# Kernel tuning notes

Hardware: AMD Instinct MI355X
Metric: run time of the kernel (lower is better)

The kernel has to match this reference:

```python
import jax, jax.numpy as jnp
import numpy as np

N_NODES = 50000
N_EDGES = 800000
IN_C = 128
OUT_C = 128
ALPHA = 0.2  # leaky_relu negative slope (args.egat_alpha)
EDGE_K = 3   # edgefeat width, fixed by W_out in-dim = 3*out_channels


def setup_inputs() -> dict:
    key = jax.random.key(0)
    k = jax.random.split(key, 7)
    h = jax.random.normal(k[0], (N_NODES, IN_C), dtype=jnp.float32)
    edge_index = jax.random.randint(k[1], (2, N_EDGES), 0, N_NODES, dtype=jnp.int64)
    edgefeat = jax.random.uniform(k[2], (N_EDGES, EDGE_K), dtype=jnp.float32)
    # glorot-initialized linear weights (stored as [in, out] for x @ W)
    def glorot(kk, fan_in, fan_out):
        lim = jnp.sqrt(6.0 / (fan_in + fan_out)).astype(jnp.float32)
        return jax.random.uniform(kk, (fan_in, fan_out), jnp.float32, -lim, lim)
    W = glorot(k[3], IN_C, OUT_C)
    a1 = glorot(k[4], OUT_C, 1)
    a2 = glorot(k[5], OUT_C, 1)
    W_out = glorot(k[6], EDGE_K * OUT_C, OUT_C)
    return {"h": h, "edge_index": edge_index, "edgefeat": edgefeat,
            "W": W, "a1": a1, "a2": a2, "W_out": W_out}


def reference(h, edge_index, edgefeat, W, a1, a2, W_out):
    src = edge_index[0]  # j: message source
    dst = edge_index[1]  # i: aggregation target
    n = h.shape[0]

    Wh = h @ W                                   # [N, C]
    s1 = Wh @ a1                                 # [N, 1] alpha_j scores
    s2 = Wh @ a2                                 # [N, 1] alpha_i scores

    # edge_update: leaky_relu(alpha_j + alpha_i) * edge_attr, then edge softmax over dst
    e = s1[src] + s2[dst]                        # [E, 1]
    e = jnp.where(e >= 0, e, ALPHA * e)
    alpha = e * edgefeat                         # [E, 3]
    m = jax.ops.segment_max(alpha, dst, num_segments=n)      # [N, 3]
    m = jnp.where(jnp.isfinite(m), m, 0.0)
    ex = jnp.exp(alpha - m[dst])
    denom = jax.ops.segment_sum(ex, dst, num_segments=n)     # [N, 3]
    att = ex / (denom[dst] + 1e-16)              # [E, 3] (dropout p applied at eval -> identity)

    # message: outer product att[E,3] x x_j[E,C] -> [E, 3C] -> W_out -> [E, C]
    x_j = Wh[src]                                # [E, C]
    msg = (att[:, :, None] * x_j[:, None, :]).reshape(att.shape[0], EDGE_K * Wh.shape[1])
    msg = msg @ W_out                            # [E, C]

    # aggregate: sum at destination nodes
    out = jax.ops.segment_sum(msg, dst, num_segments=n)      # [N, C]
    return out
```

## Files before the change

kernel.cpp:

```cpp
#include <hip/hip_runtime.h>
#include <hip/hip_bf16.h>

#define ALPHA 0.2f
typedef unsigned int uint32;
typedef __attribute__((ext_vector_type(8))) short short8;
typedef __attribute__((ext_vector_type(4))) float f32x4;

static __device__ __forceinline__ unsigned short f2bf(float f) {
    unsigned int u = __float_as_uint(f);
    u += 0x7fffu + ((u >> 16) & 1u);
    return (unsigned short)(u >> 16);
}
static __device__ __forceinline__ uint32 pk2bf(float lo, float hi) {
    return (uint32)f2bf(lo) | ((uint32)f2bf(hi) << 16);
}
static __device__ __forceinline__ float bflo(uint32 u) { return __uint_as_float(u << 16); }
static __device__ __forceinline__ float bfhi(uint32 u) { return __uint_as_float(u & 0xffff0000u); }

__global__ __launch_bounds__(256) void k1_hist_prep(const int* __restrict__ ei,
                                                    int* __restrict__ counts,
                                                    int* __restrict__ eslot, int E,
                                                    const float* __restrict__ W,
                                                    const float* __restrict__ Wout,
                                                    const float* __restrict__ a1,
                                                    const float* __restrict__ a2,
                                                    unsigned short* __restrict__ WT2,
                                                    float* __restrict__ w1f,
                                                    float* __restrict__ w2f, int nbh) {
    __shared__ float Wos[128 * 16];
    const int tid = threadIdx.x;
    if ((int)blockIdx.x < nbh) {
        int e = blockIdx.x * 256 + tid;
        if (e < E) eslot[e] = atomicAdd(&counts[ei[E + e]], 1);
        return;
    }
    int bp = blockIdx.x - nbh;
    if (bp < 24) {
        int s = bp >> 3, nb = bp & 7;
        for (int i = tid; i < 2048; i += 256) {
            int c = i >> 4, q = i & 15;
            Wos[i] = Wout[(size_t)(s * 128 + c) * 128 + nb * 16 + q];
        }
        __syncthreads();
        int j = tid & 127, nh = tid >> 7;
        float acc[8];
#pragma unroll
        for (int p = 0; p < 8; ++p) acc[p] = 0.f;
        for (int c = 0; c < 128; ++c) {
            float w = W[j * 128 + c];
#pragma unroll
            for (int p = 0; p < 8; ++p) acc[p] += w * Wos[c * 16 + nh * 8 + p];
        }
#pragma unroll
        for (int p = 0; p < 8; ++p) {
            int n = nb * 16 + nh * 8 + p;
            WT2[((size_t)s * 128 + n) * 128 + j] = f2bf(acc[p]);
        }
    } else {
        if (tid < 128) {
            float acc1 = 0.f, acc2 = 0.f;
            for (int c = 0; c < 128; ++c) {
                float w = W[tid * 128 + c];
                acc1 += w * a1[c];
                acc2 += w * a2[c];
            }
            w1f[tid] = acc1;
            w2f[tid] = acc2;
        }
    }
}

__global__ __launch_bounds__(256) void k2_mmy_scan(const float* __restrict__ h,
                                                   const unsigned short* __restrict__ WT2,
                                                   const float* __restrict__ w1f,
                                                   const float* __restrict__ w2f,
                                                   unsigned short* __restrict__ Yb,
                                                   float* __restrict__ s1,
                                                   float* __restrict__ s2, int M,
                                                   const int* __restrict__ counts,
                                                   int* __restrict__ rowptr,
                                                   int N, int E, int nbm) {
    __shared__ unsigned short As[64 * 128];
    __shared__ unsigned short Bs[128 * 128];
    __shared__ float ws1[128], ws2[128];
    __shared__ int wsums[4];
    __shared__ int base_s;
    const int tid = threadIdx.x;

    if ((int)blockIdx.x >= nbm) {
        const int bs   = blockIdx.x - nbm;
        const int lane = tid & 63, wv = tid >> 6;
        const int limit = bs * 1024;
        int acc = 0;
        for (int i = tid * 4; i < limit; i += 1024) {
            int4 v = *(const int4*)(counts + i);
            acc += v.x + v.y + v.z + v.w;
        }
#pragma unroll
        for (int off = 32; off > 0; off >>= 1) acc += __shfl_down(acc, off);
        if (lane == 0) wsums[wv] = acc;
        __syncthreads();
        if (tid == 0) base_s = wsums[0] + wsums[1] + wsums[2] + wsums[3];
        __syncthreads();
        int i0 = bs * 1024 + tid * 4;
        int v0 = 0, v1 = 0, v2 = 0, v3 = 0;
        if (i0 + 3 < N) {
            int4 v = *(const int4*)(counts + i0);
            v0 = v.x; v1 = v.y; v2 = v.z; v3 = v.w;
        } else {
            if (i0 + 0 < N) v0 = counts[i0 + 0];
            if (i0 + 1 < N) v1 = counts[i0 + 1];
            if (i0 + 2 < N) v2 = counts[i0 + 2];
            if (i0 + 3 < N) v3 = counts[i0 + 3];
        }
        int tt = v0 + v1 + v2 + v3;
        int incl = tt;
#pragma unroll
        for (int off = 1; off < 64; off <<= 1) {
            int t = __shfl_up(incl, off);
            if (lane >= off) incl += t;
        }
        __syncthreads();
        if (lane == 63) wsums[wv] = incl;
        __syncthreads();
        int woff = 0;
        for (int w2 = 0; w2 < wv; ++w2) woff += wsums[w2];
        int base = base_s + woff + (incl - tt);
        if (i0 + 0 < N) rowptr[i0 + 0] = base;
        if (i0 + 1 < N) rowptr[i0 + 1] = base + v0;
        if (i0 + 2 < N) rowptr[i0 + 2] = base + v0 + v1;
        if (i0 + 3 < N) rowptr[i0 + 3] = base + v0 + v1 + v2;
        if (bs == 0 && tid == 0) rowptr[N] = E;
        return;
    }

    const int lane = tid & 63;
    const int w    = tid >> 6;
    const int row0 = blockIdx.x * 64;

    if (tid < 128) ws1[tid] = w1f[tid];
    else           ws2[tid - 128] = w2f[tid - 128];
    __syncthreads();

    const float4* h4 = (const float4*)h;
    float sp1[4], sp2[4];
#pragma unroll
    for (int m = 0; m < 4; ++m) { sp1[m] = 0.f; sp2[m] = 0.f; }
#pragma unroll
    for (int m = 0; m < 4; ++m) {
        int i = m * 256 + tid;
        int r = i >> 4, g = i & 15;
        int rg = row0 + r;
        float4 va = make_float4(0.f, 0.f, 0.f, 0.f), vb = va;
        if (rg < M) {
            va = h4[(size_t)rg * 32 + g * 2];
            vb = h4[(size_t)rg * 32 + g * 2 + 1];
        }
        float4 wa1 = *(const float4*)(ws1 + g * 8);
        float4 wb1 = *(const float4*)(ws1 + g * 8 + 4);
        float4 wa2 = *(const float4*)(ws2 + g * 8);
        float4 wb2 = *(const float4*)(ws2 + g * 8 + 4);
        sp1[m] += va.x * wa1.x + va.y * wa1.y + va.z * wa1.z + va.w * wa1.w
                + vb.x * wb1.x + vb.y * wb1.y + vb.z * wb1.z + vb.w * wb1.w;
        sp2[m] += va.x * wa2.x + va.y * wa2.y + va.z * wa2.z + va.w * wa2.w
                + vb.x * wb2.x + vb.y * wb2.y + vb.z * wb2.z + vb.w * wb2.w;
        uint4 u;
        u.x = pk2bf(va.x, va.y); u.y = pk2bf(va.z, va.w);
        u.z = pk2bf(vb.x, vb.y); u.w = pk2bf(vb.z, vb.w);
        *(uint4*)(As + r * 128 + ((g ^ (r & 15)) * 8)) = u;
    }
#pragma unroll
    for (int m = 0; m < 4; ++m) {
#pragma unroll
        for (int off = 1; off < 16; off <<= 1) {
            sp1[m] += __shfl_xor(sp1[m], off);
            sp2[m] += __shfl_xor(sp2[m], off);
        }
    }
    if ((tid & 15) == 0) {
#pragma unroll
        for (int m = 0; m < 4; ++m) {
            int rg = row0 + m * 16 + (tid >> 4);
            if (rg < M) { s1[rg] = sp1[m]; s2[rg] = sp2[m]; }
        }
    }

    const int ml   = lane & 15;
    const int quad = lane >> 4;
    for (int ks = 0; ks < 3; ++ks) {
        __syncthreads();
#pragma unroll
        for (int m = 0; m < 8; ++m) {
            int i = m * 256 + tid;
            int n = i >> 4, g = i & 15;
            uint4 v = *(const uint4*)(WT2 + (size_t)ks * 16384 + n * 128 + g * 8);
            *(uint4*)(Bs + n * 128 + ((g ^ (n & 15)) * 8)) = v;
        }
        __syncthreads();

        f32x4 acc[8];
#pragma unroll
        for (int nt = 0; nt < 8; ++nt) acc[nt] = (f32x4){0.f, 0.f, 0.f, 0.f};
#pragma unroll
        for (int kc = 0; kc < 4; ++kc) {
            int gl = ((kc * 4 + quad) ^ ml) * 8;
            short8 af = *(const short8*)(As + (w * 16 + ml) * 128 + gl);
#pragma unroll
            for (int nt = 0; nt < 8; ++nt) {
                short8 bf = *(const short8*)(Bs + (nt * 16 + ml) * 128 + gl);
                acc[nt] = __builtin_amdgcn_mfma_f32_16x16x32_bf16(af, bf, acc[nt], 0, 0, 0);
            }
        }
        int rbase = row0 + w * 16 + quad * 4;
#pragma unroll
        for (int r = 0; r < 4; ++r) {
            int rg = rbase + r;
            if (rg >= M) continue;
            unsigned short* yrow = Yb + (size_t)rg * 384 + ks * 128 + ml;
#pragma unroll
            for (int nt = 0; nt < 8; ++nt)
                yrow[nt * 16] = f2bf(acc[nt][r]);
        }
    }
}

__global__ __launch_bounds__(256) void scatter_kernel(const int* __restrict__ ei,
                                                      const float* __restrict__ ef,
                                                      const float* __restrict__ s1,
                                                      const float* __restrict__ s2,
                                                      const int* __restrict__ rowptr,
                                                      const int* __restrict__ eslot,
                                                      float4* __restrict__ rec, int E) {
    int e = blockIdx.x * blockDim.x + threadIdx.x;
    if (e >= E) return;
    int src = ei[e];
    int dst = ei[E + e];
    float s = s1[src] + s2[dst];
    s = (s >= 0.f) ? s : ALPHA * s;
    float ex0 = __expf(s * ef[e * 3 + 0]);
    float ex1 = __expf(s * ef[e * 3 + 1]);
    float ex2 = __expf(s * ef[e * 3 + 2]);
    int pos = rowptr[dst] + eslot[e];
    rec[pos] = make_float4(ex0, ex1, ex2, __int_as_float(src));
}

__global__ __launch_bounds__(256) void agg_kernel(const float4* __restrict__ rec,
                                                  const int* __restrict__ rowptr,
                                                  const uint32* __restrict__ Yu,
                                                  float* __restrict__ out, int N) {
    int node = (blockIdx.x * blockDim.x + threadIdx.x) >> 6;
    int lane = threadIdx.x & 63;
    if (node >= N) return;
    int beg = rowptr[node], end = rowptr[node + 1];

    float d0 = 0.f, d1 = 0.f, d2 = 0.f;
    for (int jb = beg + lane; jb < end; jb += 64) {
        float4 r = rec[jb];
        d0 += r.x; d1 += r.y; d2 += r.z;
    }
#pragma unroll
    for (int off = 32; off > 0; off >>= 1) {
        d0 += __shfl_xor(d0, off);
        d1 += __shfl_xor(d1, off);
        d2 += __shfl_xor(d2, off);
    }
    float inv0 = 1.f / (d0 + 1e-16f);
    float inv1 = 1.f / (d1 + 1e-16f);
    float inv2 = 1.f / (d2 + 1e-16f);

    float a0 = 0.f, a1 = 0.f;
    int j = beg;
    for (; j + 3 < end; j += 4) {
        float4 r0 = rec[j], r1 = rec[j + 1], r2 = rec[j + 2], r3 = rec[j + 3];
        const uint32* p0 = Yu + (size_t)__float_as_int(r0.w) * 192;
        const uint32* p1 = Yu + (size_t)__float_as_int(r1.w) * 192;
        const uint32* p2 = Yu + (size_t)__float_as_int(r2.w) * 192;
        const uint32* p3 = Yu + (size_t)__float_as_int(r3.w) * 192;
        uint32 u00 = p0[lane], u01 = p0[64 + lane], u02 = p0[128 + lane];
        uint32 u10 = p1[lane], u11 = p1[64 + lane], u12 = p1[128 + lane];
        uint32 u20 = p2[lane], u21 = p2[64 + lane], u22 = p2[128 + lane];
        uint32 u30 = p3[lane], u31 = p3[64 + lane], u32 = p3[128 + lane];
        float w00 = r0.x * inv0, w01 = r0.y * inv1, w02 = r0.z * inv2;
        float w10 = r1.x * inv0, w11 = r1.y * inv1, w12 = r1.z * inv2;
        float w20 = r2.x * inv0, w21 = r2.y * inv1, w22 = r2.z * inv2;
        float w30 = r3.x * inv0, w31 = r3.y * inv1, w32 = r3.z * inv2;
        a0 += w00 * bflo(u00) + w01 * bflo(u01) + w02 * bflo(u02);
        a1 += w00 * bfhi(u00) + w01 * bfhi(u01) + w02 * bfhi(u02);
        a0 += w10 * bflo(u10) + w11 * bflo(u11) + w12 * bflo(u12);
        a1 += w10 * bfhi(u10) + w11 * bfhi(u11) + w12 * bfhi(u12);
        a0 += w20 * bflo(u20) + w21 * bflo(u21) + w22 * bflo(u22);
        a1 += w20 * bfhi(u20) + w21 * bfhi(u21) + w22 * bfhi(u22);
        a0 += w30 * bflo(u30) + w31 * bflo(u31) + w32 * bflo(u32);
        a1 += w30 * bfhi(u30) + w31 * bfhi(u31) + w32 * bfhi(u32);
    }
    for (; j < end; ++j) {
        float4 r0 = rec[j];
        const uint32* p0 = Yu + (size_t)__float_as_int(r0.w) * 192;
        uint32 u00 = p0[lane], u01 = p0[64 + lane], u02 = p0[128 + lane];
        float w00 = r0.x * inv0, w01 = r0.y * inv1, w02 = r0.z * inv2;
        a0 += w00 * bflo(u00) + w01 * bflo(u01) + w02 * bflo(u02);
        a1 += w00 * bfhi(u00) + w01 * bfhi(u01) + w02 * bfhi(u02);
    }
    ((float2*)(out + (size_t)node * 128))[lane] = make_float2(a0, a1);
}

extern "C" void kernel_launch(void* const* d_in, const int* in_sizes, int n_in,
                              void* d_out, int out_size, void* d_ws, size_t ws_size,
                              hipStream_t stream) {
    const float* h    = (const float*)d_in[0];
    const int*   ei   = (const int*)d_in[1];
    const float* ef   = (const float*)d_in[2];
    const float* W    = (const float*)d_in[3];
    const float* a1   = (const float*)d_in[4];
    const float* a2   = (const float*)d_in[5];
    const float* Wout = (const float*)d_in[6];
    float*       out  = (float*)d_out;

    const int N = in_sizes[0] / 128;
    const int E = in_sizes[2] / 3;
    const int nchunk = (N + 1023) / 1024;
    const int nbh    = (E + 255) / 256;
    const int nbm    = (N + 63) / 64;

    float4* rec = (float4*)d_ws;
    unsigned short* Yb  = (unsigned short*)(rec + E);
    unsigned short* WT2 = Yb + (size_t)N * 384;
    float* w1f  = (float*)(WT2 + 3 * 128 * 128);
    float* w2f  = w1f + 128;
    float* s1   = w2f + 128;
    float* s2   = s1 + N;
    int* counts = (int*)(s2 + N);
    int* rowptr = counts + N;
    int* eslot  = rowptr + N + 1;

    (void)hipMemsetAsync(counts, 0, (size_t)N * sizeof(int), stream);

    k1_hist_prep<<<nbh + 25, 256, 0, stream>>>(ei, counts, eslot, E,
                                               W, Wout, a1, a2, WT2, w1f, w2f, nbh);
    k2_mmy_scan<<<nbm + nchunk, 256, 0, stream>>>(h, WT2, w1f, w2f, Yb, s1, s2, N,
                                                  counts, rowptr, N, E, nbm);
    scatter_kernel<<<(E + 255) / 256, 256, 0, stream>>>(ei, ef, s1, s2, rowptr, eslot, rec, E);
    agg_kernel<<<(N * 64 + 255) / 256, 256, 0, stream>>>(rec, rowptr, (const uint32*)Yb, out, N);
}
```

Before: 258.4 us.

## Pack edge records into 8 bytes and stage GEMM output through LDS

Edge records shrink from a 16-byte float4 to an 8-byte uint2. Each record holds a 17-bit source index and three 15-bit bf16 exp values with the sign bit dropped, which is safe because exp is non-negative. This halves record traffic in the scatter and aggregate kernels. The GEMM epilogue now writes its bf16 tile to shared memory first and then stores it to Y as coalesced 16-byte rows instead of scattered 2-byte writes. The cost is lower precision on the attention weights, a source-index limit of 2^17, and two extra barriers.

```diff
diff --git a/kernel.cpp b/kernel.cpp
--- a/kernel.cpp
+++ b/kernel.cpp
@@ -211,15 +211,23 @@
                 acc[nt] = __builtin_amdgcn_mfma_f32_16x16x32_bf16(af, bf, acc[nt], 0, 0, 0);
             }
         }
-        int rbase = row0 + w * 16 + quad * 4;
-#pragma unroll
-        for (int r = 0; r < 4; ++r) {
-            int rg = rbase + r;
-            if (rg >= M) continue;
-            unsigned short* yrow = Yb + (size_t)rg * 384 + ks * 128 + ml;
+        __syncthreads();
+        unsigned short* Ct = Bs;
+        int lrow = w * 16 + quad * 4;
+#pragma unroll
+        for (int r = 0; r < 4; ++r)
 #pragma unroll
             for (int nt = 0; nt < 8; ++nt)
-                yrow[nt * 16] = f2bf(acc[nt][r]);
+                Ct[(lrow + r) * 136 + nt * 16 + ml] = f2bf(acc[nt][r]);
+        __syncthreads();
+#pragma unroll
+        for (int m = 0; m < 4; ++m) {
+            int i = m * 256 + tid;
+            int r2 = i >> 4, g = i & 15;
+            int rg = row0 + r2;
+            uint4 v = *(const uint4*)(Ct + r2 * 136 + g * 8);
+            if (rg < M)
+                *(uint4*)(Yb + (size_t)rg * 384 + ks * 128 + g * 8) = v;
         }
     }
 }
@@ -230,21 +238,24 @@
                                                       const float* __restrict__ s2,
                                                       const int* __restrict__ rowptr,
                                                       const int* __restrict__ eslot,
-                                                      float4* __restrict__ rec, int E) {
+                                                      uint2* __restrict__ rec8, int E) {
     int e = blockIdx.x * blockDim.x + threadIdx.x;
     if (e >= E) return;
     int src = ei[e];
     int dst = ei[E + e];
     float s = s1[src] + s2[dst];
     s = (s >= 0.f) ? s : ALPHA * s;
-    float ex0 = __expf(s * ef[e * 3 + 0]);
-    float ex1 = __expf(s * ef[e * 3 + 1]);
-    float ex2 = __expf(s * ef[e * 3 + 2]);
+    unsigned short b0 = f2bf(__expf(s * ef[e * 3 + 0]));
+    unsigned short b1 = f2bf(__expf(s * ef[e * 3 + 1]));
+    unsigned short b2 = f2bf(__expf(s * ef[e * 3 + 2]));
+    uint2 rv;
+    rv.x = (uint32)src | ((uint32)(b0 & 0x7fffu) << 17);
+    rv.y = (uint32)(b1 & 0x7fffu) | ((uint32)(b2 & 0x7fffu) << 15);
     int pos = rowptr[dst] + eslot[e];
-    rec[pos] = make_float4(ex0, ex1, ex2, __int_as_float(src));
-}
-
-__global__ __launch_bounds__(256) void agg_kernel(const float4* __restrict__ rec,
+    rec8[pos] = rv;
+}
+
+__global__ __launch_bounds__(256) void agg_kernel(const uint2* __restrict__ rec8,
                                                   const int* __restrict__ rowptr,
                                                   const uint32* __restrict__ Yu,
                                                   float* __restrict__ out, int N) {
@@ -255,8 +266,10 @@
 
     float d0 = 0.f, d1 = 0.f, d2 = 0.f;
     for (int jb = beg + lane; jb < end; jb += 64) {
-        float4 r = rec[jb];
-        d0 += r.x; d1 += r.y; d2 += r.z;
+        uint2 r = rec8[jb];
+        d0 += __uint_as_float((r.x >> 1) & 0x7fff0000u);
+        d1 += __uint_as_float((r.y << 16) & 0x7fff0000u);
+        d2 += __uint_as_float((r.y << 1) & 0x7fff0000u);
     }
 #pragma unroll
     for (int off = 32; off > 0; off >>= 1) {
@@ -271,19 +284,27 @@
     float a0 = 0.f, a1 = 0.f;
     int j = beg;
     for (; j + 3 < end; j += 4) {
-        float4 r0 = rec[j], r1 = rec[j + 1], r2 = rec[j + 2], r3 = rec[j + 3];
-        const uint32* p0 = Yu + (size_t)__float_as_int(r0.w) * 192;
-        const uint32* p1 = Yu + (size_t)__float_as_int(r1.w) * 192;
-        const uint32* p2 = Yu + (size_t)__float_as_int(r2.w) * 192;
-        const uint32* p3 = Yu + (size_t)__float_as_int(r3.w) * 192;
+        uint2 r0 = rec8[j], r1 = rec8[j + 1], r2 = rec8[j + 2], r3 = rec8[j + 3];
+        const uint32* p0 = Yu + (size_t)(r0.x & 0x1ffffu) * 192;
+        const uint32* p1 = Yu + (size_t)(r1.x & 0x1ffffu) * 192;
+        const uint32* p2 = Yu + (size_t)(r2.x & 0x1ffffu) * 192;
+        const uint32* p3 = Yu + (size_t)(r3.x & 0x1ffffu) * 192;
         uint32 u00 = p0[lane], u01 = p0[64 + lane], u02 = p0[128 + lane];
         uint32 u10 = p1[lane], u11 = p1[64 + lane], u12 = p1[128 + lane];
         uint32 u20 = p2[lane], u21 = p2[64 + lane], u22 = p2[128 + lane];
         uint32 u30 = p3[lane], u31 = p3[64 + lane], u32 = p3[128 + lane];
-        float w00 = r0.x * inv0, w01 = r0.y * inv1, w02 = r0.z * inv2;
-        float w10 = r1.x * inv0, w11 = r1.y * inv1, w12 = r1.z * inv2;
-        float w20 = r2.x * inv0, w21 = r2.y * inv1, w22 = r2.z * inv2;
-        float w30 = r3.x * inv0, w31 = r3.y * inv1, w32 = r3.z * inv2;
+        float w00 = __uint_as_float((r0.x >> 1) & 0x7fff0000u) * inv0;
+        float w01 = __uint_as_float((r0.y << 16) & 0x7fff0000u) * inv1;
+        float w02 = __uint_as_float((r0.y << 1) & 0x7fff0000u) * inv2;
+        float w10 = __uint_as_float((r1.x >> 1) & 0x7fff0000u) * inv0;
+        float w11 = __uint_as_float((r1.y << 16) & 0x7fff0000u) * inv1;
+        float w12 = __uint_as_float((r1.y << 1) & 0x7fff0000u) * inv2;
+        float w20 = __uint_as_float((r2.x >> 1) & 0x7fff0000u) * inv0;
+        float w21 = __uint_as_float((r2.y << 16) & 0x7fff0000u) * inv1;
+        float w22 = __uint_as_float((r2.y << 1) & 0x7fff0000u) * inv2;
+        float w30 = __uint_as_float((r3.x >> 1) & 0x7fff0000u) * inv0;
+        float w31 = __uint_as_float((r3.y << 16) & 0x7fff0000u) * inv1;
+        float w32 = __uint_as_float((r3.y << 1) & 0x7fff0000u) * inv2;
         a0 += w00 * bflo(u00) + w01 * bflo(u01) + w02 * bflo(u02);
         a1 += w00 * bfhi(u00) + w01 * bfhi(u01) + w02 * bfhi(u02);
         a0 += w10 * bflo(u10) + w11 * bflo(u11) + w12 * bflo(u12);
@@ -294,10 +315,12 @@
         a1 += w30 * bfhi(u30) + w31 * bfhi(u31) + w32 * bfhi(u32);
     }
     for (; j < end; ++j) {
-        float4 r0 = rec[j];
-        const uint32* p0 = Yu + (size_t)__float_as_int(r0.w) * 192;
+        uint2 r0 = rec8[j];
+        const uint32* p0 = Yu + (size_t)(r0.x & 0x1ffffu) * 192;
         uint32 u00 = p0[lane], u01 = p0[64 + lane], u02 = p0[128 + lane];
-        float w00 = r0.x * inv0, w01 = r0.y * inv1, w02 = r0.z * inv2;
+        float w00 = __uint_as_float((r0.x >> 1) & 0x7fff0000u) * inv0;
+        float w01 = __uint_as_float((r0.y << 16) & 0x7fff0000u) * inv1;
+        float w02 = __uint_as_float((r0.y << 1) & 0x7fff0000u) * inv2;
         a0 += w00 * bflo(u00) + w01 * bflo(u01) + w02 * bflo(u02);
         a1 += w00 * bfhi(u00) + w01 * bfhi(u01) + w02 * bfhi(u02);
     }
@@ -322,8 +345,8 @@
     const int nbh    = (E + 255) / 256;
     const int nbm    = (N + 63) / 64;
 
-    float4* rec = (float4*)d_ws;
-    unsigned short* Yb  = (unsigned short*)(rec + E);
+    uint2* rec8 = (uint2*)d_ws;
+    unsigned short* Yb  = (unsigned short*)(rec8 + E);
     unsigned short* WT2 = Yb + (size_t)N * 384;
     float* w1f  = (float*)(WT2 + 3 * 128 * 128);
     float* w2f  = w1f + 128;
@@ -339,6 +362,6 @@
                                                W, Wout, a1, a2, WT2, w1f, w2f, nbh);
     k2_mmy_scan<<<nbm + nchunk, 256, 0, stream>>>(h, WT2, w1f, w2f, Yb, s1, s2, N,
                                                   counts, rowptr, N, E, nbm);
-    scatter_kernel<<<(E + 255) / 256, 256, 0, stream>>>(ei, ef, s1, s2, rowptr, eslot, rec, E);
-    agg_kernel<<<(N * 64 + 255) / 256, 256, 0, stream>>>(rec, rowptr, (const uint32*)Yb, out, N);
-}
+    scatter_kernel<<<(E + 255) / 256, 256, 0, stream>>>(ei, ef, s1, s2, rowptr, eslot, rec8, E);
+    agg_kernel<<<(N * 64 + 255) / 256, 256, 0, stream>>>(rec8, rowptr, (const uint32*)Yb, out, N);
+}
```

Measured after the change: 248.8 us. 3.7% less time.
